# Kernel tuning notes

Measured on AMD Instinct MI355X. Metric: run time of the kernel, lower is better.

The kernel has to match this reference:

```python
import jax, jax.numpy as jnp
import numpy as np

N_NODES = 50000
N_EDGES = 1600000
IN_CH = 128
HID = 32
HEADS = 3
OUT_CH = 32
NEG_SLOPE = 0.2


def setup_inputs() -> dict:
    key = jax.random.key(0)
    ks = jax.random.split(key, 12)
    s = 0.05
    x = jax.random.normal(ks[0], (N_NODES, IN_CH), dtype=jnp.float32)
    edge_index = jax.random.randint(ks[1], (2, N_EDGES), 0, N_NODES, dtype=jnp.int64)
    W1 = jax.random.normal(ks[2], (IN_CH, HEADS * HID), dtype=jnp.float32) * s
    att_src1 = jax.random.normal(ks[3], (HEADS, HID), dtype=jnp.float32) * s
    att_dst1 = jax.random.normal(ks[4], (HEADS, HID), dtype=jnp.float32) * s
    b1 = jnp.zeros((HEADS * HID,), dtype=jnp.float32)
    W2 = jax.random.normal(ks[5], (HEADS * HID, OUT_CH), dtype=jnp.float32) * s
    att_src2 = jax.random.normal(ks[6], (1, OUT_CH), dtype=jnp.float32) * s
    att_dst2 = jax.random.normal(ks[7], (1, OUT_CH), dtype=jnp.float32) * s
    b2 = jnp.zeros((OUT_CH,), dtype=jnp.float32)
    Wp = jax.random.normal(ks[8], (OUT_CH, 1), dtype=jnp.float32) * s
    bp = jnp.zeros((1,), dtype=jnp.float32)
    return dict(x=x, edge_index=edge_index, W1=W1, att_src1=att_src1,
                att_dst1=att_dst1, b1=b1, W2=W2, att_src2=att_src2,
                att_dst2=att_dst2, b2=b2, Wp=Wp, bp=bp)


def gat_layer(x, src, dst, W, a_src, a_dst, b, heads, out_ch, concat):
    # PyG GATConv semantics: per-head linear, edge attention with leaky_relu,
    # softmax over incoming edges per destination node, scatter-add aggregate.
    N = x.shape[0]
    h = (x @ W).reshape(N, heads, out_ch)                 # [N,H,C]
    a_s = jnp.einsum('nhc,hc->nh', h, a_src)              # [N,H]
    a_d = jnp.einsum('nhc,hc->nh', h, a_dst)              # [N,H]
    e = jax.nn.leaky_relu(a_s[src] + a_d[dst], NEG_SLOPE) # [E,H]
    m = jax.ops.segment_max(e, dst, num_segments=N)       # stable softmax per dst
    p = jnp.exp(e - m[dst])
    s = jax.ops.segment_sum(p, dst, num_segments=N)
    alpha = p / (s[dst] + 1e-16)                          # [E,H]
    msg = h[src] * alpha[:, :, None]                      # [E,H,C]
    out = jax.ops.segment_sum(msg, dst, num_segments=N)   # [N,H,C]
    out = out.reshape(N, heads * out_ch) if concat else out.mean(axis=1)
    return out + b


def reference(x, edge_index, W1, att_src1, att_dst1, b1, W2, att_src2,
              att_dst2, b2, Wp, bp):
    N = x.shape[0]
    loop = jnp.arange(N, dtype=edge_index.dtype)
    src = jnp.concatenate([edge_index[0], loop])  # add self-loops (PyG default)
    dst = jnp.concatenate([edge_index[1], loop])
    h = gat_layer(x, src, dst, W1, att_src1, att_dst1, b1, HEADS, HID, True)
    h = jax.nn.elu(h)
    h = gat_layer(h, src, dst, W2, att_src2, att_dst2, b2, 1, OUT_CH, False)
    prob = jax.nn.sigmoid(h @ Wp + bp)                    # [N,1]
    return prob
```

## Files before the change

### kernel.cpp

```cpp
#include <hip/hip_runtime.h>
#include <hip/hip_bf16.h>
#include <math.h>


#define IN_CH 128
#define HID 32
#define HEADS 3
#define OUT_CH 32
#define NEG_SLOPE 0.2f

#define NBUCK_SHIFT 6
#define NBUCK_NODES 64
#define BCAP 2560
#define EPB 4096

typedef unsigned int uint;
typedef unsigned short ushort;
typedef short v8s __attribute__((ext_vector_type(8)));
typedef float v4f __attribute__((ext_vector_type(4)));
typedef uint v3u __attribute__((ext_vector_type(3)));

static __device__ __forceinline__ uint f2bf(float f) {
    uint u = __float_as_uint(f);
    return (u + 0x7FFFu + ((u >> 16) & 1u)) >> 16;
}
static __device__ __forceinline__ uint pk4fp8(float a, float b, float c, float d) {
    int r = 0;
    r = __builtin_amdgcn_cvt_pk_fp8_f32(a, b, r, false);
    r = __builtin_amdgcn_cvt_pk_fp8_f32(c, d, r, true);
    return (uint)r;
}
static __device__ __forceinline__ float elu_f(float o) {
    return o > 0.f ? o : __expf(o) - 1.f;
}
static __device__ __forceinline__ float frcp(float x) {
    return __builtin_amdgcn_rcpf(x);
}

#define LDA 136
#define LDC 100


__global__ __launch_bounds__(256) void k_pre(const float* __restrict__ W1,
                                             ushort* __restrict__ w1t,
                                             int* __restrict__ gcur) {
    int b = blockIdx.x, t = threadIdx.x;
    if (b < 12) {
        int base = b * 1024 + t * 4;
        #pragma unroll
        for (int j = 0; j < 4; ++j) {
            int idx = base + j;
            int n = idx >> 7, k = idx & 127;
            w1t[idx] = (ushort)f2bf(W1[k * 96 + n]);
        }
    } else {
        int i = (b - 12) * 256 + t;
        if (i < 1024) gcur[i] = 0;
    }
}


__global__ __launch_bounds__(256) void k_g1b(const float* __restrict__ x,
                                             const ushort* __restrict__ w1t,
                                             const float* __restrict__ as,
                                             const float* __restrict__ ad,
                                             uint* __restrict__ h1u,
                                             float* __restrict__ a_d1p,
                                             const int* __restrict__ ei,
                                             int E, int Etot, int B2, int G1,
                                             int* __restrict__ gcur,
                                             uint* __restrict__ stage, int N) {
    __shared__ __attribute__((aligned(16))) char raw[64 * LDC * 4];
    int tid = threadIdx.x;

    if ((int)blockIdx.x >= G1) {
        int* hist     = (int*)raw;
        int* runStart = hist + 1024;
        int* rankCtr  = runStart + 1024;
        for (int i = tid; i < 1024; i += 256) { hist[i] = 0; rankCtr[i] = 0; }
        __syncthreads();
        int base = ((int)blockIdx.x - G1) * EPB;

        uint rec[16];
        #pragma unroll
        for (int i = 0; i < 16; ++i) {
            int e = base + tid + i * 256;
            uint r = 0xFFFFFFFFu;
            if (e < Etot) {
                int s, d;
                if (e < E) { s = ei[e]; d = ei[E + e]; }
                else       { s = e - E; d = s; }
                r = ((uint)d << 16) | (uint)s;
                atomicAdd(&hist[d >> NBUCK_SHIFT], 1);
            }
            rec[i] = r;
        }
        __syncthreads();
        for (int i = tid; i < B2; i += 256) {
            int c = hist[i];
            if (c) runStart[i] = atomicAdd(&gcur[i], c);
        }
        __syncthreads();
        #pragma unroll
        for (int i = 0; i < 16; ++i) {
            uint r = rec[i];
            if (r != 0xFFFFFFFFu) {
                int b = (int)(r >> 16) >> NBUCK_SHIFT;
                int pos = runStart[b] + atomicAdd(&rankCtr[b], 1);
                if (pos < BCAP)
                    stage[(size_t)b * BCAP + pos] = r & 0x003FFFFFu;
            }
        }
        return;
    }

    ushort* sA  = (ushort*)raw;
    float*  sC  = (float*)raw;
    int b0 = blockIdx.x * 64;

    uint* sA32 = (uint*)sA;
    #pragma unroll
    for (int i = 0; i < 8; ++i) {
        int g = tid + i * 256;
        int row = g >> 5, c4 = g & 31;
        float4 v = make_float4(0.f, 0.f, 0.f, 0.f);
        int gn = b0 + row;
        if (gn < N) v = *(const float4*)(x + (size_t)gn * IN_CH + c4 * 4);
        sA32[row * 68 + c4 * 2]     = f2bf(v.x) | (f2bf(v.y) << 16);
        sA32[row * 68 + c4 * 2 + 1] = f2bf(v.z) | (f2bf(v.w) << 16);
    }
    __syncthreads();

    int l = tid & 63, w = tid >> 6;
    int m15 = l & 15, q = l >> 4;

    v8s afr[4];
    const ushort* arow = sA + (w * 16 + m15) * LDA + q * 8;
    #pragma unroll
    for (int kc = 0; kc < 4; ++kc) afr[kc] = *(const v8s*)(arow + kc * 32);

    v4f acc[6];
    #pragma unroll
    for (int cg = 0; cg < 6; ++cg) {
        acc[cg] = (v4f){0.f, 0.f, 0.f, 0.f};
        const ushort* browg = w1t + (cg * 16 + m15) * 128 + q * 8;
        #pragma unroll
        for (int kc = 0; kc < 4; ++kc) {
            v8s bfr = *(const v8s*)(browg + kc * 32);
            acc[cg] = __builtin_amdgcn_mfma_f32_16x16x32_bf16(afr[kc], bfr, acc[cg], 0, 0, 0);
        }
    }
    __syncthreads();
    #pragma unroll
    for (int cg = 0; cg < 6; ++cg) {
        int col = cg * 16 + m15;
        #pragma unroll
        for (int r = 0; r < 4; ++r)
            sC[(w * 16 + q * 4 + r) * LDC + col] = acc[cg][r];
    }
    __syncthreads();

    if (tid < 192) {
        int ln = tid / 3, h = tid - ln * 3;
        int node = b0 + ln;
        if (node < N) {
            const float* vs = as + h * 32;
            const float* vd = ad + h * 32;
            const float* row = sC + ln * LDC + h * 32;
            float4 s4 = make_float4(0.f, 0.f, 0.f, 0.f);
            float4 d4 = make_float4(0.f, 0.f, 0.f, 0.f);
            #pragma unroll
            for (int c = 0; c < 8; ++c) {
                float4 r = *(const float4*)(row + 4 * c);
                float4 a = *(const float4*)(vs + 4 * c);
                float4 bb = *(const float4*)(vd + 4 * c);
                s4.x += r.x * a.x;  s4.y += r.y * a.y;
                s4.z += r.z * a.z;  s4.w += r.w * a.w;
                d4.x += r.x * bb.x; d4.y += r.y * bb.y;
                d4.z += r.z * bb.z; d4.w += r.w * bb.w;
            }
            float s = (s4.x + s4.y) + (s4.z + s4.w);
            float d = (d4.x + d4.y) + (d4.z + d4.w);
            ((float*)h1u)[(size_t)node * 32 + 24 + h] = s;
            a_d1p[node * 4 + h] = d;
        }
    }
    {
        int node = tid >> 2, part = tid & 3;
        int gn = b0 + node;
        if (gn < N) {
            const float* row = sC + node * LDC;
            uint tmp[6];
            #pragma unroll
            for (int jj = 0; jj < 6; ++jj) {
                int j = part * 6 + jj;
                int dd = j / 3, slot = j - dd * 3;
                const float* p = row + slot * 32 + dd * 4;
                tmp[jj] = pk4fp8(p[0], p[1], p[2], p[3]);
            }
            uint* dst = h1u + (size_t)gn * 32 + part * 6;
            *(uint2*)(dst + 0) = make_uint2(tmp[0], tmp[1]);
            *(uint2*)(dst + 2) = make_uint2(tmp[2], tmp[3]);
            *(uint2*)(dst + 4) = make_uint2(tmp[4], tmp[5]);
        }
    }
}


__global__ __launch_bounds__(256) void k_sort(const uint* __restrict__ stage,
                                              const int* __restrict__ gcur,
                                              int* __restrict__ offs,
                                              ushort* __restrict__ edges,
                                              int N, int Etot, int B2) {
    __shared__ uint items[BCAP];
    __shared__ int red[256];
    __shared__ int lofs[NBUCK_NODES + 1];
    __shared__ int cursors[NBUCK_NODES];
    int t = threadIdx.x;
    int b = blockIdx.x;

    int partial = 0;
    for (int i = t; i < b; i += 256) partial += gcur[i];
    red[t] = partial;
    if (t < NBUCK_NODES) cursors[t] = 0;
    __syncthreads();
    #pragma unroll
    for (int s = 128; s > 0; s >>= 1) {
        if (t < s) red[t] += red[t + s];
        __syncthreads();
    }
    int gbase = red[0];
    int cnt = gcur[b]; if (cnt > BCAP) cnt = BCAP;

    for (int i = t; i < cnt; i += 256) items[i] = stage[(size_t)b * BCAP + i];
    __syncthreads();
    for (int i = t; i < cnt; i += 256) atomicAdd(&cursors[items[i] >> 16], 1);
    __syncthreads();
    if (t == 0) {
        int run = 0;
        for (int i = 0; i < NBUCK_NODES; ++i) { int v = cursors[i]; lofs[i] = run; run += v; }
        lofs[NBUCK_NODES] = run;
    }
    __syncthreads();
    int nodeBase = b << NBUCK_SHIFT;
    if (t < NBUCK_NODES && nodeBase + t < N) offs[nodeBase + t] = gbase + lofs[t];
    if (b == B2 - 1 && t == 0) offs[N] = Etot;
    if (t < NBUCK_NODES) cursors[t] = 0;
    __syncthreads();
    for (int i = t; i < cnt; i += 256) {
        uint it = items[i];
        int ln = (int)(it >> 16);
        int r = atomicAdd(&cursors[ln], 1);
        edges[gbase + lofs[ln] + r] = (ushort)(it & 0xFFFFu);
    }
}


#define W2LD 36

__global__ __launch_bounds__(256) void k_agg1g2(const int* __restrict__ offs,
                                                const ushort* __restrict__ edges,
                                                const uint* __restrict__ h1u,
                                                const float* __restrict__ a_d1p,
                                                const float* __restrict__ b1,
                                                const float* __restrict__ W2,
                                                const float* __restrict__ as2,
                                                const float* __restrict__ ad2,
                                                uint* __restrict__ h2u,
                                                float* __restrict__ a_d2, int N) {
    __shared__ __attribute__((aligned(16))) float sW2[96 * W2LD];
    __shared__ float ss2[32], sd2[32];
    __shared__ float rowbuf[16][96];

    int tid = threadIdx.x;
    #pragma unroll
    for (int i = 0; i < 3; ++i) {
        int gg = tid + i * 256;
        int k = gg >> 3, c4i = gg & 7;
        *(float4*)&sW2[k * W2LD + c4i * 4] = *(const float4*)(W2 + k * 32 + c4i * 4);
    }
    if (tid < 32) { ss2[tid] = as2[tid]; sd2[tid] = ad2[tid]; }
    __syncthreads();

    int w = tid >> 6;
    int lane = tid & 63;
    int grp = lane >> 4, hl = lane & 15;
    int node = blockIdx.x * 16 + w * 4 + grp;
    bool nvalid = node < N;
    int nodeC = nvalid ? node : (N - 1);
    int g = hl >> 3, d = hl & 7;
    const float4 adv = *(const float4*)(a_d1p + nodeC * 4);

    int off0 = offs[nodeC], off1 = offs[nodeC + 1];
    int deg = off1 - off0;
    if (deg < 0) deg = 0;
    int nIt = (deg + 1) >> 1;
    int o16 = __shfl_xor(nIt, 16); nIt = nIt > o16 ? nIt : o16;
    int o32 = __shfl_xor(nIt, 32); int itMax = nIt > o32 ? nIt : o32;

    float a00 = 0.f, a01 = 0.f, a02 = 0.f, a03 = 0.f;
    float a10 = 0.f, a11 = 0.f, a12 = 0.f, a13 = 0.f;
    float a20 = 0.f, a21 = 0.f, a22 = 0.f, a23 = 0.f;
    float d0 = 0.f, d1 = 0.f, d2 = 0.f;

    #pragma unroll 2
    for (int i = 0; i < itMax; ++i) {
        int e = i * 2 + g;
        bool act = e < deg;
        int eidx = off0 + (act ? e : 0);
        uint src = (uint)edges[eidx];
        const uint* hr = h1u + src * 32u;
        float4 af = *(const float4*)(hr + 24);
        v3u wv = *(const v3u*)(hr + 3 * d);
        float z0 = af.x + adv.x, z1 = af.y + adv.y, z2 = af.z + adv.z;
        z0 = fmaxf(z0, NEG_SLOPE * z0);
        z1 = fmaxf(z1, NEG_SLOPE * z1);
        z2 = fmaxf(z2, NEG_SLOPE * z2);
        float p0 = __expf(z0), p1 = __expf(z1), p2 = __expf(z2);
        p0 = act ? p0 : 0.f;
        p1 = act ? p1 : 0.f;
        p2 = act ? p2 : 0.f;
        { auto lo = __builtin_amdgcn_cvt_pk_f32_fp8((int)wv[0], false);
          auto hi = __builtin_amdgcn_cvt_pk_f32_fp8((int)wv[0], true);
          a00 += p0 * lo[0]; a01 += p0 * lo[1];
          a02 += p0 * hi[0]; a03 += p0 * hi[1]; }
        { auto lo = __builtin_amdgcn_cvt_pk_f32_fp8((int)wv[1], false);
          auto hi = __builtin_amdgcn_cvt_pk_f32_fp8((int)wv[1], true);
          a10 += p1 * lo[0]; a11 += p1 * lo[1];
          a12 += p1 * hi[0]; a13 += p1 * hi[1]; }
        { auto lo = __builtin_amdgcn_cvt_pk_f32_fp8((int)wv[2], false);
          auto hi = __builtin_amdgcn_cvt_pk_f32_fp8((int)wv[2], true);
          a20 += p2 * lo[0]; a21 += p2 * lo[1];
          a22 += p2 * hi[0]; a23 += p2 * hi[1]; }
        d0 += p0; d1 += p1; d2 += p2;
    }

    #define REDF(v) { v += __shfl_xor(v, 8); }
    REDF(a00) REDF(a01) REDF(a02) REDF(a03)
    REDF(a10) REDF(a11) REDF(a12) REDF(a13)
    REDF(a20) REDF(a21) REDF(a22) REDF(a23)
    REDF(d0) REDF(d1) REDF(d2)
    #undef REDF

    int rbrow = w * 4 + grp;
    if (hl < 8) {
        float r0 = frcp(d0 + 1e-16f);
        float r1 = frcp(d1 + 1e-16f);
        float r2 = frcp(d2 + 1e-16f);
        float4 bv0 = *(const float4*)(b1 + 4 * hl);
        float4 bv1 = *(const float4*)(b1 + 32 + 4 * hl);
        float4 bv2 = *(const float4*)(b1 + 64 + 4 * hl);
        float4 v;
        v.x = elu_f(a00 * r0 + bv0.x);
        v.y = elu_f(a01 * r0 + bv0.y);
        v.z = elu_f(a02 * r0 + bv0.z);
        v.w = elu_f(a03 * r0 + bv0.w);
        *(float4*)&rowbuf[rbrow][4 * hl] = v;
        v.x = elu_f(a10 * r1 + bv1.x);
        v.y = elu_f(a11 * r1 + bv1.y);
        v.z = elu_f(a12 * r1 + bv1.z);
        v.w = elu_f(a13 * r1 + bv1.w);
        *(float4*)&rowbuf[rbrow][32 + 4 * hl] = v;
        v.x = elu_f(a20 * r2 + bv2.x);
        v.y = elu_f(a21 * r2 + bv2.y);
        v.z = elu_f(a22 * r2 + bv2.z);
        v.w = elu_f(a23 * r2 + bv2.w);
        *(float4*)&rowbuf[rbrow][64 + 4 * hl] = v;
    }

    int c4 = hl & 7, kg = hl >> 3;
    float4 accv = make_float4(0.f, 0.f, 0.f, 0.f);
    const float* rb = &rowbuf[rbrow][kg * 48];
    const float* wb = &sW2[kg * 48 * W2LD + c4 * 4];
    #pragma unroll
    for (int i = 0; i < 48; ++i) {
        float rv = rb[i];
        float4 wvv = *(const float4*)(wb + i * W2LD);
        accv.x += rv * wvv.x; accv.y += rv * wvv.y;
        accv.z += rv * wvv.z; accv.w += rv * wvv.w;
    }
    accv.x += __shfl_xor(accv.x, 8);
    accv.y += __shfl_xor(accv.y, 8);
    accv.z += __shfl_xor(accv.z, 8);
    accv.w += __shfl_xor(accv.w, 8);

    float4 sv = *(const float4*)&ss2[c4 * 4];
    float4 dv = *(const float4*)&sd2[c4 * 4];
    float ps = accv.x * sv.x + accv.y * sv.y + accv.z * sv.z + accv.w * sv.w;
    float pd = accv.x * dv.x + accv.y * dv.y + accv.z * dv.z + accv.w * dv.w;
    ps += __shfl_xor(ps, 1); ps += __shfl_xor(ps, 2); ps += __shfl_xor(ps, 4);
    pd += __shfl_xor(pd, 1); pd += __shfl_xor(pd, 2); pd += __shfl_xor(pd, 4);
    if (nvalid && hl < 8) {
        h2u[(size_t)node * 16 + c4] = pk4fp8(accv.x, accv.y, accv.z, accv.w);
        if (hl == 0) {
            ((float*)h2u)[(size_t)node * 16 + 8] = ps;
            a_d2[node] = pd;
        }
    }
}


__global__ __launch_bounds__(256) void k_agg2f(const int* __restrict__ offs,
                                               const ushort* __restrict__ edges,
                                               const uint* __restrict__ h2u,
                                               const float* __restrict__ a_d2,
                                               const float* __restrict__ b2,
                                               const float* __restrict__ Wp,
                                               const float* __restrict__ bp,
                                               float* __restrict__ out, int N) {
    int tid = threadIdx.x;
    int w = tid >> 6;
    int lane = tid & 63;
    int grp = lane >> 4, hl = lane & 15;
    int node = blockIdx.x * 16 + w * 4 + grp;
    bool nvalid = node < N;
    int nodeC = nvalid ? node : (N - 1);
    int g = hl >> 3, d = hl & 7;
    const float ad2u = a_d2[nodeC];

    int off0 = offs[nodeC], off1 = offs[nodeC + 1];
    int deg = off1 - off0;
    if (deg < 0) deg = 0;
    int nIt = (deg + 1) >> 1;
    int o16 = __shfl_xor(nIt, 16); nIt = nIt > o16 ? nIt : o16;
    int o32 = __shfl_xor(nIt, 32); int itMax = nIt > o32 ? nIt : o32;

    float c0 = 0.f, c1 = 0.f, c2 = 0.f, c3 = 0.f, den = 0.f;

    #pragma unroll 2
    for (int i = 0; i < itMax; ++i) {
        int e = i * 2 + g;
        bool act = e < deg;
        int eidx = off0 + (act ? e : 0);
        uint src = (uint)edges[eidx];
        const uint* hr = h2u + src * 16u;
        float zf = *(const float*)(hr + 8);
        uint wvv = hr[d];
        float z = zf + ad2u;
        z = fmaxf(z, NEG_SLOPE * z);
        float p = __expf(z);
        p = act ? p : 0.f;
        auto lo = __builtin_amdgcn_cvt_pk_f32_fp8((int)wvv, false);
        auto hi = __builtin_amdgcn_cvt_pk_f32_fp8((int)wvv, true);
        c0 += p * lo[0]; c1 += p * lo[1];
        c2 += p * hi[0]; c3 += p * hi[1];
        den += p;
    }

    #define REDF(v) { v += __shfl_xor(v, 8); }
    REDF(c0) REDF(c1) REDF(c2) REDF(c3) REDF(den)
    #undef REDF

    float4 bv = *(const float4*)(b2 + 4 * d);
    float4 wv = *(const float4*)(Wp + 4 * d);
    float r = frcp(den + 1e-16f);
    float v = (c0 * r + bv.x) * wv.x + (c1 * r + bv.y) * wv.y +
              (c2 * r + bv.z) * wv.z + (c3 * r + bv.w) * wv.w;
    v += __shfl_xor(v, 1);
    v += __shfl_xor(v, 2);
    v += __shfl_xor(v, 4);
    if (nvalid && hl == 0)
        out[node] = frcp(1.f + __expf(-(v + bp[0])));
}


extern "C" void kernel_launch(void* const* d_in, const int* in_sizes, int n_in,
                              void* d_out, int out_size, void* d_ws, size_t ws_size,
                              hipStream_t stream) {
    const float* x      = (const float*)d_in[0];
    const int*   ei     = (const int*)d_in[1];
    const float* W1     = (const float*)d_in[2];
    const float* att_s1 = (const float*)d_in[3];
    const float* att_d1 = (const float*)d_in[4];
    const float* b1     = (const float*)d_in[5];
    const float* W2     = (const float*)d_in[6];
    const float* att_s2 = (const float*)d_in[7];
    const float* att_d2 = (const float*)d_in[8];
    const float* b2     = (const float*)d_in[9];
    const float* Wp     = (const float*)d_in[10];
    const float* bp     = (const float*)d_in[11];
    float* out = (float*)d_out;

    const int N = in_sizes[0] / IN_CH;
    const int E = in_sizes[1] / 2;
    const int Etot = E + N;
    const int B2 = (N + NBUCK_NODES - 1) >> NBUCK_SHIFT;
    const int G1 = (N + 63) / 64;
    const int BK = (Etot + EPB - 1) / EPB;

    float*  ws    = (float*)d_ws;
    uint*   h1u   = (uint*)ws;
    float*  a_d1p = ws + (size_t)N * 32;
    int*    offs  = (int*)(a_d1p + (size_t)N * 4);
    ushort* edges = (ushort*)(offs + (N + 1));
    int*    gcur  = (int*)(edges + (((size_t)Etot + 1) & ~(size_t)1));
    uint*   stage = (uint*)(gcur + 1024);
    uint*   h2u   = stage + (size_t)B2 * BCAP;
    float*  a_d2  = (float*)(h2u + (size_t)N * 16);
    ushort* w1t   = (ushort*)(a_d2 + N);

    k_pre<<<16, 256, 0, stream>>>(W1, w1t, gcur);

    k_g1b<<<G1 + BK, 256, 0, stream>>>(x, w1t, att_s1, att_d1, h1u, a_d1p,
                                       ei, E, Etot, B2, G1, gcur, stage, N);
    k_sort<<<B2, 256, 0, stream>>>(stage, gcur, offs, edges, N, Etot, B2);

    k_agg1g2<<<(N + 15) / 16, 256, 0, stream>>>(offs, edges, h1u, a_d1p, b1, W2,
                                                att_s2, att_d2, h2u, a_d2, N);
    k_agg2f<<<(N + 15) / 16, 256, 0, stream>>>(offs, edges, h2u, a_d2,
                                               b2, Wp, bp, out, N);
}
```

Baseline: 195.9 us.

## Replace global bucket-cursor atomics with per-block prefix histograms for edge staging

The binning blocks now do a local prefix scan of their bucket histogram and write edges into a per-block contiguous staging region, recording per-block offsets in a global histogram table. Cross-block coordination then needs only a bucket-total atomic instead of atomics that return position cursors. The sort kernel gathers each bucket's pieces from all staging blocks using the stored offsets. This removes the ordering dependence on returned atomic values and makes staging writes more local, but sort blocks now read a BK-wide histogram column and copy many small runs serially per thread.

```diff
diff --git a/kernel.cpp b/kernel.cpp
--- a/kernel.cpp
+++ b/kernel.cpp
@@ -43,7 +43,7 @@
 
 __global__ __launch_bounds__(256) void k_pre(const float* __restrict__ W1,
                                              ushort* __restrict__ w1t,
-                                             int* __restrict__ gcur) {
+                                             int* __restrict__ btot) {
     int b = blockIdx.x, t = threadIdx.x;
     if (b < 12) {
         int base = b * 1024 + t * 4;
@@ -55,7 +55,7 @@
         }
     } else {
         int i = (b - 12) * 256 + t;
-        if (i < 1024) gcur[i] = 0;
+        if (i < 1024) btot[i] = 0;
     }
 }
 
@@ -68,18 +68,20 @@
                                              float* __restrict__ a_d1p,
                                              const int* __restrict__ ei,
                                              int E, int Etot, int B2, int G1,
-                                             int* __restrict__ gcur,
+                                             int* __restrict__ btot,
+                                             int* __restrict__ bhist,
                                              uint* __restrict__ stage, int N) {
     __shared__ __attribute__((aligned(16))) char raw[64 * LDC * 4];
     int tid = threadIdx.x;
 
     if ((int)blockIdx.x >= G1) {
-        int* hist     = (int*)raw;
-        int* runStart = hist + 1024;
-        int* rankCtr  = runStart + 1024;
-        for (int i = tid; i < 1024; i += 256) { hist[i] = 0; rankCtr[i] = 0; }
+        int* hist  = (int*)raw;
+        int* rankc = hist + 1024;
+        int* part  = rankc + 1024;
+        for (int i = tid; i < 1024; i += 256) { hist[i] = 0; rankc[i] = 0; }
         __syncthreads();
-        int base = ((int)blockIdx.x - G1) * EPB;
+        int blk = (int)blockIdx.x - G1;
+        int base = blk * EPB;
 
         uint rec[16];
         #pragma unroll
@@ -96,19 +98,40 @@
             rec[i] = r;
         }
         __syncthreads();
-        for (int i = tid; i < B2; i += 256) {
-            int c = hist[i];
-            if (c) runStart[i] = atomicAdd(&gcur[i], c);
-        }
+        int c0 = hist[tid * 4 + 0], c1 = hist[tid * 4 + 1];
+        int c2 = hist[tid * 4 + 2], c3 = hist[tid * 4 + 3];
+        int lsum = c0 + c1 + c2 + c3;
+        part[tid] = lsum;
         __syncthreads();
+        for (int off = 1; off < 256; off <<= 1) {
+            int v = (tid >= off) ? part[tid - off] : 0;
+            __syncthreads();
+            part[tid] += v;
+            __syncthreads();
+        }
+        int bse = part[tid] - lsum;
+        int l0 = bse, l1 = l0 + c0, l2 = l1 + c1, l3 = l2 + c2;
+        hist[tid * 4 + 0] = l0;
+        hist[tid * 4 + 1] = l1;
+        hist[tid * 4 + 2] = l2;
+        hist[tid * 4 + 3] = l3;
+        if (c0) atomicAdd(&btot[tid * 4 + 0], c0);
+        if (c1) atomicAdd(&btot[tid * 4 + 1], c1);
+        if (c2) atomicAdd(&btot[tid * 4 + 2], c2);
+        if (c3) atomicAdd(&btot[tid * 4 + 3], c3);
+        __syncthreads();
+        #pragma unroll
+        for (int i = 0; i < 4; ++i) {
+            int q = tid + i * 256;
+            bhist[(size_t)blk * 1024 + q] = hist[q];
+        }
         #pragma unroll
         for (int i = 0; i < 16; ++i) {
             uint r = rec[i];
             if (r != 0xFFFFFFFFu) {
                 int b = (int)(r >> 16) >> NBUCK_SHIFT;
-                int pos = runStart[b] + atomicAdd(&rankCtr[b], 1);
-                if (pos < BCAP)
-                    stage[(size_t)b * BCAP + pos] = r & 0x003FFFFFu;
+                int pos = hist[b] + atomicAdd(&rankc[b], 1);
+                stage[(size_t)blk * EPB + pos] = r & 0x003FFFFFu;
             }
         }
         return;
@@ -208,21 +231,30 @@
 
 
 __global__ __launch_bounds__(256) void k_sort(const uint* __restrict__ stage,
-                                              const int* __restrict__ gcur,
+                                              const int* __restrict__ bhist,
+                                              const int* __restrict__ btot,
                                               int* __restrict__ offs,
                                               ushort* __restrict__ edges,
-                                              int N, int Etot, int B2) {
+                                              int N, int Etot, int B2, int BK) {
     __shared__ uint items[BCAP];
+    __shared__ int soff[416], scnt[416], spre[416];
     __shared__ int red[256];
     __shared__ int lofs[NBUCK_NODES + 1];
     __shared__ int cursors[NBUCK_NODES];
+    __shared__ int stot;
     int t = threadIdx.x;
     int b = blockIdx.x;
 
     int partial = 0;
-    for (int i = t; i < b; i += 256) partial += gcur[i];
+    for (int i = t; i < b; i += 256) partial += btot[i];
     red[t] = partial;
     if (t < NBUCK_NODES) cursors[t] = 0;
+    for (int blk = t; blk < BK; blk += 256) {
+        const int* row = bhist + (size_t)blk * 1024;
+        int o = row[b], nx = row[b + 1];
+        soff[blk] = o;
+        scnt[blk] = nx - o;
+    }
     __syncthreads();
     #pragma unroll
     for (int s = 128; s > 0; s >>= 1) {
@@ -230,11 +262,22 @@
         __syncthreads();
     }
     int gbase = red[0];
-    int cnt = gcur[b]; if (cnt > BCAP) cnt = BCAP;
-
-    for (int i = t; i < cnt; i += 256) items[i] = stage[(size_t)b * BCAP + i];
-    __syncthreads();
-    for (int i = t; i < cnt; i += 256) atomicAdd(&cursors[items[i] >> 16], 1);
+    if (t == 0) {
+        int run = 0;
+        for (int i = 0; i < BK; ++i) { spre[i] = run; run += scnt[i]; }
+        stot = run > BCAP ? BCAP : run;
+    }
+    __syncthreads();
+    int total = stot;
+
+    for (int cell = t; cell < BK; cell += 256) {
+        int c = scnt[cell], p0 = spre[cell];
+        const uint* sp = stage + (size_t)cell * EPB + soff[cell];
+        for (int j = 0; j < c; ++j)
+            if (p0 + j < BCAP) items[p0 + j] = sp[j];
+    }
+    __syncthreads();
+    for (int i = t; i < total; i += 256) atomicAdd(&cursors[items[i] >> 16], 1);
     __syncthreads();
     if (t == 0) {
         int run = 0;
@@ -247,7 +290,7 @@
     if (b == B2 - 1 && t == 0) offs[N] = Etot;
     if (t < NBUCK_NODES) cursors[t] = 0;
     __syncthreads();
-    for (int i = t; i < cnt; i += 256) {
+    for (int i = t; i < total; i += 256) {
         uint it = items[i];
         int ln = (int)(it >> 16);
         int r = atomicAdd(&cursors[ln], 1);
@@ -493,17 +536,20 @@
     float*  a_d1p = ws + (size_t)N * 32;
     int*    offs  = (int*)(a_d1p + (size_t)N * 4);
     ushort* edges = (ushort*)(offs + (N + 1));
-    int*    gcur  = (int*)(edges + (((size_t)Etot + 1) & ~(size_t)1));
-    uint*   stage = (uint*)(gcur + 1024);
-    uint*   h2u   = stage + (size_t)B2 * BCAP;
+    int*    btot  = (int*)(edges + (((size_t)Etot + 1) & ~(size_t)1));
+    int*    bhist = btot + 1024;
+    uint*   stage = (uint*)(bhist + (size_t)BK * 1024);
+    uint*   h2u   = stage + (size_t)BK * EPB;
     float*  a_d2  = (float*)(h2u + (size_t)N * 16);
     ushort* w1t   = (ushort*)(a_d2 + N);
 
-    k_pre<<<16, 256, 0, stream>>>(W1, w1t, gcur);
+    k_pre<<<16, 256, 0, stream>>>(W1, w1t, btot);
 
     k_g1b<<<G1 + BK, 256, 0, stream>>>(x, w1t, att_s1, att_d1, h1u, a_d1p,
-                                       ei, E, Etot, B2, G1, gcur, stage, N);
-    k_sort<<<B2, 256, 0, stream>>>(stage, gcur, offs, edges, N, Etot, B2);
+                                       ei, E, Etot, B2, G1, btot, bhist,
+                                       stage, N);
+    k_sort<<<B2, 256, 0, stream>>>(stage, bhist, btot, offs, edges,
+                                   N, Etot, B2, BK);
 
     k_agg1g2<<<(N + 15) / 16, 256, 0, stream>>>(offs, edges, h1u, a_d1p, b1, W2,
                                                 att_s2, att_d2, h2u, a_d2, N);
```

Measured after the change: 238.3 us. +21.6%, slower.
